# Performance work log

Hardware: AMD Instinct MI355X
Metric: run time of the kernel (lower is better)

Reference implementation:

```python
import jax, jax.numpy as jnp
import numpy as np

N_NODES = 50000
N_EDGES = 640000
IN_DIM = 128
HID = 128
OUT_DIM = 16
BATCH = 2
EPS = 1e-5


def setup_inputs() -> dict:
    key = jax.random.key(0)
    ks = jax.random.split(key, 12)
    x = jax.random.normal(ks[0], (BATCH, N_NODES, IN_DIM), dtype=jnp.float32)
    edge_index = jax.random.randint(ks[1], (2, N_EDGES), 0, N_NODES, dtype=jnp.int32)
    # learned per-edge log-weights (initialized ~0 like nn.Parameter(zeros), small noise for a nontrivial test)
    edge_weight_param = 0.01 * jax.random.normal(ks[2], (N_EDGES,), dtype=jnp.float32)
    s1 = 1.0 / np.sqrt(IN_DIM)
    s2 = 1.0 / np.sqrt(HID)
    W1 = jax.random.uniform(ks[3], (IN_DIM, HID), minval=-s1, maxval=s1, dtype=jnp.float32)
    b1 = jnp.zeros((HID,), jnp.float32)
    W2 = jax.random.uniform(ks[4], (HID, HID), minval=-s2, maxval=s2, dtype=jnp.float32)
    b2 = jnp.zeros((HID,), jnp.float32)
    g1 = jnp.ones((HID,), jnp.float32); be1 = jnp.zeros((HID,), jnp.float32)
    g2 = jnp.ones((HID,), jnp.float32); be2 = jnp.zeros((HID,), jnp.float32)
    Wc = jax.random.uniform(ks[5], (HID, OUT_DIM), minval=-s2, maxval=s2, dtype=jnp.float32)
    bc = jax.random.uniform(ks[6], (OUT_DIM,), minval=-s2, maxval=s2, dtype=jnp.float32)
    return {"x": x, "edge_index": edge_index, "edge_weight_param": edge_weight_param,
            "W1": W1, "b1": b1, "W2": W2, "b2": b2,
            "g1": g1, "be1": be1, "g2": g2, "be2": be2,
            "Wc": Wc, "bc": bc}


def _gcn_norm(edge_index, edge_weight):
    # PyG GCNConv: add self-loops (weight 1), symmetric D^-1/2 A D^-1/2 normalization
    row = jnp.concatenate([edge_index[0], jnp.arange(N_NODES, dtype=edge_index.dtype)])
    col = jnp.concatenate([edge_index[1], jnp.arange(N_NODES, dtype=edge_index.dtype)])
    ew = jnp.concatenate([edge_weight, jnp.ones((N_NODES,), edge_weight.dtype)])
    deg = jax.ops.segment_sum(ew, col, num_segments=N_NODES)
    dinv = jnp.where(deg > 0, jax.lax.rsqrt(jnp.maximum(deg, 1e-30)), 0.0)
    norm = dinv[row] * ew * dinv[col]
    return row, col, norm


def _gcn_conv(x, W, b, row, col, norm):
    # x: [B, N, F_in] -> [B, N, F_out]; gather-scale-scatter over edges
    xw = x @ W                                   # [B, N, H]
    msg = xw[:, row, :] * norm[None, :, None]    # [B, E+N, H]
    out = jax.vmap(lambda m: jax.ops.segment_sum(m, col, num_segments=N_NODES))(msg)
    return out + b


def _batchnorm(h, gamma, beta):
    # training-mode BN over flattened (B*N) rows, biased variance, eps=1e-5
    B, N, F = h.shape
    hf = h.reshape(-1, F)
    mu = hf.mean(axis=0)
    var = hf.var(axis=0)
    return (((hf - mu) * jax.lax.rsqrt(var + EPS)) * gamma + beta).reshape(B, N, F)


def reference(x, edge_index, edge_weight_param, W1, b1, W2, b2, g1, be1, g2, be2, Wc, bc):
    edge_weight = jnp.exp(edge_weight_param)  # learned exp edge weights
    row, col, norm = _gcn_norm(edge_index, edge_weight)
    h = jax.nn.relu(_gcn_conv(x, W1, b1, row, col, norm))
    h = _batchnorm(h, g1, be1)
    # dropout is identity in eval / deterministic reference
    h = jax.nn.relu(_gcn_conv(h, W2, b2, row, col, norm))
    h = _batchnorm(h, g2, be2)
    return h @ Wc + bc  # [B, N, OUT_DIM]
```

## Files before the change

### kernel.cpp

```cpp
#include <hip/hip_runtime.h>
#include <hip/hip_bf16.h>
#include <cstdint>
#include <cstddef>

#define N_NODES 50000
#define N_EDGES 640000
#define ROWS    100000
#define HID     128
#define OUTD    16
#define AGG_BLOCKS 2048
#define MID_BLOCKS 32
#define SCAN_BLOCKS 196
#define GEMM_BLOCKS 512
#define G2_BLOCKS   800
#define GEMM_TILES  (ROWS / 16)
#define PAIR_TILES  (N_NODES / 16)
#define EG_BLOCKS   3500
#define EG_GEMM_WAVES 4000

typedef __attribute__((ext_vector_type(8))) uint16_t ushort8;
typedef __attribute__((ext_vector_type(8))) __bf16   bf16x8;
typedef __attribute__((ext_vector_type(4))) float    floatx4;

union FragU { ushort8 u; bf16x8 b; };

__device__ __forceinline__ float bf_lo(uint32_t u){
  union { uint32_t u; float f; } c; c.u = u << 16; return c.f;
}
__device__ __forceinline__ float bf_hi(uint32_t u){
  union { uint32_t u; float f; } c; c.u = u & 0xffff0000u; return c.f;
}
__device__ __forceinline__ uint16_t f2bf(float f){
  union { float f; uint32_t u; } c; c.f = f;
  uint32_t u = c.u;
  uint32_t r = (u + 0x7fffu + ((u >> 16) & 1u)) >> 16;
  return (uint16_t)r;
}

__device__ __forceinline__ void pack_w(int t, const float* __restrict__ W,
                                       const float* sca ,
                                       uint16_t* __restrict__ WP){
  int L = t & 63;
  int s = (t >> 6) & 3;
  int c = t >> 8;
  int n = (c >> 1) * 32 + 2 * (L & 15) + (c & 1);
  int k0 = s * 32 + (L >> 4) * 8;
  ushort8 r;
#pragma unroll
  for (int j = 0; j < 8; j++){
    float w = W[(size_t)(k0 + j) * HID + n];
    if (sca) w *= sca[k0 + j];
    r[j] = f2bf(w);
  }
  *((ushort8*)(WP + (size_t)t * 8)) = r;
}

__global__ void k_initpack(unsigned long long* __restrict__ dc,
                           const float* __restrict__ W1, uint16_t* __restrict__ WP1){
  int b = blockIdx.x;
  if (b < SCAN_BLOCKS){
    int i = b * 256 + threadIdx.x;
    if (i < N_NODES) dc[i] = 0ull;
  } else {
    pack_w((b - SCAN_BLOCKS) * 256 + threadIdx.x, W1, nullptr, WP1);
  }
}

__global__ __launch_bounds__(256, 2) void k_edge_gemm1(const int* __restrict__ ei,
                                                       const float* __restrict__ ewp,
                                                       unsigned long long* __restrict__ dc,
                                                       unsigned int* __restrict__ slot,
                                                       const float* __restrict__ X,
                                                       const uint16_t* __restrict__ WP,
                                                       uint16_t* __restrict__ Y){
  const int b = blockIdx.x;
  const int g = b % 7;
  if (g < 5){
    const int eb = (b / 7) * 5 + g;
    const int e = eb * 256 + threadIdx.x;
    float w = expf(ewp[e]);
    int c = ei[N_EDGES + e];
    unsigned long long inc = (1ull << 44) | (unsigned long long)(w * 1048576.0f + 0.5f);
    unsigned long long old = atomicAdd(&dc[c], inc);
    slot[e] = (unsigned int)(old >> 44);
    return;
  }
  const int lane = threadIdx.x & 63;
  const int wid  = threadIdx.x >> 6;
  const int gw   = ((b / 7) * 2 + (g - 5)) * 4 + wid;
  const int m    = lane & 15;
  const int kq   = lane >> 4;

  FragU wf[8][4];
#pragma unroll
  for (int c = 0; c < 8; c++)
#pragma unroll
    for (int s = 0; s < 4; s++)
      wf[c][s].u = *((const ushort8*)(WP + (size_t)(((c * 4 + s) * 64 + lane) * 8)));

  unsigned long long* Yq = (unsigned long long*)Y;
  for (int t = gw; t < PAIR_TILES; t += EG_GEMM_WAVES){
    const int nb = t * 16;
    uint32_t pr0[16];
    {
      FragU af[4];
#pragma unroll
      for (int s = 0; s < 4; s++){
        const float* p = X + (size_t)(nb + m) * HID + s * 32 + kq * 8;
        floatx4 f0 = *((const floatx4*)p);
        floatx4 f1 = *((const floatx4*)(p + 4));
        ushort8 r;
#pragma unroll
        for (int j = 0; j < 4; j++){ r[j] = f2bf(f0[j]); r[j + 4] = f2bf(f1[j]); }
        af[s].u = r;
      }
      floatx4 acc[8];
#pragma unroll
      for (int c = 0; c < 8; c++) acc[c] = floatx4{0.f, 0.f, 0.f, 0.f};
#pragma unroll
      for (int s = 0; s < 4; s++)
#pragma unroll
        for (int c = 0; c < 8; c++)
          acc[c] = __builtin_amdgcn_mfma_f32_16x16x32_bf16(af[s].b, wf[c][s].b, acc[c], 0, 0, 0);
#pragma unroll
      for (int t4 = 0; t4 < 4; t4++)
#pragma unroll
        for (int i = 0; i < 4; i++)
          pr0[t4 * 4 + i] = (uint32_t)f2bf(acc[2 * t4][i]) | ((uint32_t)f2bf(acc[2 * t4 + 1][i]) << 16);
    }
    {
      FragU af[4];
#pragma unroll
      for (int s = 0; s < 4; s++){
        const float* p = X + (size_t)(N_NODES + nb + m) * HID + s * 32 + kq * 8;
        floatx4 f0 = *((const floatx4*)p);
        floatx4 f1 = *((const floatx4*)(p + 4));
        ushort8 r;
#pragma unroll
        for (int j = 0; j < 4; j++){ r[j] = f2bf(f0[j]); r[j + 4] = f2bf(f1[j]); }
        af[s].u = r;
      }
      floatx4 acc[8];
#pragma unroll
      for (int c = 0; c < 8; c++) acc[c] = floatx4{0.f, 0.f, 0.f, 0.f};
#pragma unroll
      for (int s = 0; s < 4; s++)
#pragma unroll
        for (int c = 0; c < 8; c++)
          acc[c] = __builtin_amdgcn_mfma_f32_16x16x32_bf16(af[s].b, wf[c][s].b, acc[c], 0, 0, 0);
#pragma unroll
      for (int t4 = 0; t4 < 4; t4++)
#pragma unroll
        for (int i = 0; i < 4; i++){
          uint32_t pr1 = (uint32_t)f2bf(acc[2 * t4][i]) | ((uint32_t)f2bf(acc[2 * t4 + 1][i]) << 16);
          Yq[(size_t)(nb + kq * 4 + i) * 64 + t4 * 16 + m] =
              (unsigned long long)pr0[t4 * 4 + i] | ((unsigned long long)pr1 << 32);
        }
    }
  }
}

__global__ void k_scan_bsum(const unsigned long long* __restrict__ dc, int* __restrict__ bsum,
                            float* __restrict__ dinv){
  __shared__ int sd[256];
  int tid = threadIdx.x;
  int i = blockIdx.x * 256 + tid;
  int cnt = 0;
  if (i < N_NODES){
    unsigned long long v = dc[i];
    cnt = (int)(v >> 44);
    float deg = 1.0f + (float)((double)(v & ((1ull << 44) - 1)) * (1.0 / 1048576.0));
    dinv[i] = 1.0f / sqrtf(deg);
  }
  sd[tid] = cnt;
  __syncthreads();
  for (int off = 128; off > 0; off >>= 1){
    if (tid < off) sd[tid] += sd[tid + off];
    __syncthreads();
  }
  if (tid == 0) bsum[blockIdx.x] = sd[0];
}

__global__ void k_scan_write(const unsigned long long* __restrict__ dc, const int* __restrict__ bsum,
                             int* __restrict__ rp){
  __shared__ int sb[256];
  __shared__ int sd[256];
  int tid = threadIdx.x;
  sb[tid] = (tid < SCAN_BLOCKS && tid < blockIdx.x) ? bsum[tid] : 0;
  __syncthreads();
  for (int off = 128; off > 0; off >>= 1){
    if (tid < off) sb[tid] += sb[tid + off];
    __syncthreads();
  }
  const int base = sb[0];

  int i = blockIdx.x * 256 + tid;
  int v = (i < N_NODES) ? (int)(dc[i] >> 44) : 0;
  sd[tid] = v;
  __syncthreads();
  for (int off = 1; off < 256; off <<= 1){
    int t = (tid >= off) ? sd[tid - off] : 0;
    __syncthreads();
    sd[tid] += t;
    __syncthreads();
  }
  if (i < N_NODES) rp[i] = base + sd[tid] - v;
  if (blockIdx.x == 0 && tid == 0) rp[N_NODES] = N_EDGES;
}

__global__ void k_fill(const int* __restrict__ ei, const float* __restrict__ ewp,
                       const float* __restrict__ dinv, const unsigned int* __restrict__ slot,
                       const int* __restrict__ rp, unsigned long long* __restrict__ edg){
  int e = blockIdx.x * 256 + threadIdx.x;
  if (e < N_EDGES){
    int r = ei[e];
    int c = ei[N_EDGES + e];
    float w = expf(ewp[e]);
    float nrm = dinv[r] * w * dinv[c];
    int p = rp[c] + (int)slot[e];
    edg[p] = ((unsigned long long)__float_as_uint(nrm) << 32) | (unsigned int)r;
  }
}

__global__ __launch_bounds__(256, 2) void k_gemm2(const uint16_t* __restrict__ X,
                                                  const uint16_t* __restrict__ WP,
                                                  uint16_t* __restrict__ Y){
  const int lane = threadIdx.x & 63;
  const int wid  = threadIdx.x >> 6;
  const int gw   = blockIdx.x * 4 + wid;
  const int nw   = G2_BLOCKS * 4;
  const int m    = lane & 15;
  const int kq   = lane >> 4;

  FragU wf[8][4];
#pragma unroll
  for (int c = 0; c < 8; c++)
#pragma unroll
    for (int s = 0; s < 4; s++)
      wf[c][s].u = *((const ushort8*)(WP + (size_t)(((c * 4 + s) * 64 + lane) * 8)));

  unsigned long long* Yq = (unsigned long long*)Y;
  for (int t = gw; t < PAIR_TILES; t += nw){
    const int nb = t * 16;
    uint32_t pr0[16];
    {
      FragU af[4];
#pragma unroll
      for (int s = 0; s < 4; s++)
        af[s].u = *((const ushort8*)(X + (size_t)(nb + m) * HID + s * 32 + kq * 8));
      floatx4 acc[8];
#pragma unroll
      for (int c = 0; c < 8; c++) acc[c] = floatx4{0.f, 0.f, 0.f, 0.f};
#pragma unroll
      for (int s = 0; s < 4; s++)
#pragma unroll
        for (int c = 0; c < 8; c++)
          acc[c] = __builtin_amdgcn_mfma_f32_16x16x32_bf16(af[s].b, wf[c][s].b, acc[c], 0, 0, 0);
#pragma unroll
      for (int t4 = 0; t4 < 4; t4++)
#pragma unroll
        for (int i = 0; i < 4; i++)
          pr0[t4 * 4 + i] = (uint32_t)f2bf(acc[2 * t4][i]) | ((uint32_t)f2bf(acc[2 * t4 + 1][i]) << 16);
    }
    {
      FragU af[4];
#pragma unroll
      for (int s = 0; s < 4; s++)
        af[s].u = *((const ushort8*)(X + (size_t)(N_NODES + nb + m) * HID + s * 32 + kq * 8));
      floatx4 acc[8];
#pragma unroll
      for (int c = 0; c < 8; c++) acc[c] = floatx4{0.f, 0.f, 0.f, 0.f};
#pragma unroll
      for (int s = 0; s < 4; s++)
#pragma unroll
        for (int c = 0; c < 8; c++)
          acc[c] = __builtin_amdgcn_mfma_f32_16x16x32_bf16(af[s].b, wf[c][s].b, acc[c], 0, 0, 0);
#pragma unroll
      for (int t4 = 0; t4 < 4; t4++)
#pragma unroll
        for (int i = 0; i < 4; i++){
          uint32_t pr1 = (uint32_t)f2bf(acc[2 * t4][i]) | ((uint32_t)f2bf(acc[2 * t4 + 1][i]) << 16);
          Yq[(size_t)(nb + kq * 4 + i) * 64 + t4 * 16 + m] =
              (unsigned long long)pr0[t4 * 4 + i] | ((unsigned long long)pr1 << 32);
        }
    }
  }
}

__global__ __launch_bounds__(256) void k_cls_mfma(const uint16_t* __restrict__ H,
                                                  const uint16_t* __restrict__ WPC,
                                                  const float* __restrict__ cvec,
                                                  float* __restrict__ out){
  const int lane = threadIdx.x & 63;
  const int wid  = threadIdx.x >> 6;
  const int gw   = blockIdx.x * 4 + wid;
  const int nw   = GEMM_BLOCKS * 4;
  const int m    = lane & 15;
  const int kq   = lane >> 4;

  FragU wf[4];
#pragma unroll
  for (int s = 0; s < 4; s++)
    wf[s].u = *((const ushort8*)(WPC + (size_t)((s * 64 + lane) * 8)));
  const float cv = cvec[m];

  for (int t = gw; t < GEMM_TILES; t += nw){
    const int row0 = t * 16;
    FragU af[4];
#pragma unroll
    for (int s = 0; s < 4; s++)
      af[s].u = *((const ushort8*)(H + (size_t)(row0 + m) * HID + s * 32 + kq * 8));
    floatx4 acc = floatx4{0.f, 0.f, 0.f, 0.f};
#pragma unroll
    for (int s = 0; s < 4; s++)
      acc = __builtin_amdgcn_mfma_f32_16x16x32_bf16(af[s].b, wf[s].b, acc, 0, 0, 0);
#pragma unroll
    for (int i = 0; i < 4; i++)
      out[(size_t)(row0 + kq * 4 + i) * OUTD + m] = acc[i] + cv;
  }
}

__global__ __launch_bounds__(256) void k_agg(const uint16_t* __restrict__ XW,
                                             const int* __restrict__ rp,
                                             const unsigned long long* __restrict__ edg,
                                             const float* __restrict__ dinv,
                                             const float* __restrict__ bias,
                                             const float* __restrict__ cvec,
                                             uint16_t* __restrict__ H,
                                             float* __restrict__ psum,
                                             float* __restrict__ pssq){
  __shared__ float lsum[128];
  __shared__ float lssq[128];
  const int tid = threadIdx.x;
  if (tid < 128){ lsum[tid] = 0.f; lssq[tid] = 0.f; }
  __syncthreads();

  const int lane = tid & 63;
  const int wid  = tid >> 6;
  const int gw   = blockIdx.x * 4 + wid;
  const int nw   = AGG_BLOCKS * 4;
  const unsigned long long* Xq = (const unsigned long long*)XW;
  uint32_t* Hu = (uint32_t*)H;
  const int f0 = lane * 2;
  const float b0 = bias[f0], b1 = bias[f0 + 1];
  const float c0 = cvec ? cvec[f0] : 0.f;
  const float c1 = cvec ? cvec[f0 + 1] : 0.f;
  float ts0 = 0.f, ts1 = 0.f, tq0 = 0.f, tq1 = 0.f;
  const int lu = lane & 7;

  int node = gw;
  if (node < N_NODES){
    int e0 = rp[node], e1 = rp[node + 1];
    float di = dinv[node];
    unsigned long long sv = Xq[(size_t)node * 64 + lane];
    unsigned long long rec = 0ull;
    if (e0 < e1){
      int a = e0 + lu; if (a > N_EDGES - 1) a = N_EDGES - 1;
      rec = edg[a];
    }
    while (true){
      const int nn = node + nw;
      const bool more = (nn < N_NODES);
      int ne0 = 0, ne1 = 0; float ndi = 0.f; unsigned long long nsv = 0ull;
      if (more){
        ne0 = rp[nn]; ne1 = rp[nn + 1];
        ndi = dinv[nn];
        nsv = Xq[(size_t)nn * 64 + lane];
      }

      const float sn = di * di;
      const uint32_t s0 = (uint32_t)sv, s1 = (uint32_t)(sv >> 32);
      float a0x = sn * bf_lo(s0), a0y = sn * bf_hi(s0);
      float a1x = sn * bf_lo(s1), a1y = sn * bf_hi(s1);
      float wsum = sn;

      for (int e = e0; e < e1; e += 8){
        const int r = e1 - e;
        const uint32_t rlo = (uint32_t)rec;
        const uint32_t rhi = (uint32_t)(rec >> 32);
        const int pe = (r > 8) ? (e + 8) : (more ? ne0 : -1);
        if (pe >= 0){
          int a = pe + lu; if (a > N_EDGES - 1) a = N_EDGES - 1;
          rec = edg[a];
        }
        unsigned long long q[8];
        if (r >= 8){
#pragma unroll
          for (int u = 0; u < 8; u++)
            q[u] = Xq[(size_t)(uint32_t)__builtin_amdgcn_readlane((int)rlo, u) * 64 + lane];
#pragma unroll
          for (int u = 0; u < 8; u++){
            const float w = __uint_as_float((uint32_t)__builtin_amdgcn_readlane((int)rhi, u));
            const uint32_t g0 = (uint32_t)q[u], g1 = (uint32_t)(q[u] >> 32);
            a0x = fmaf(w, bf_lo(g0), a0x); a0y = fmaf(w, bf_hi(g0), a0y);
            a1x = fmaf(w, bf_lo(g1), a1x); a1y = fmaf(w, bf_hi(g1), a1y);
            wsum += w;
          }
        } else {
#pragma unroll
          for (int u = 0; u < 8; u++)
            if (u < r)
              q[u] = Xq[(size_t)(uint32_t)__builtin_amdgcn_readlane((int)rlo, u) * 64 + lane];
#pragma unroll
          for (int u = 0; u < 8; u++)
            if (u < r){
              const float w = __uint_as_float((uint32_t)__builtin_amdgcn_readlane((int)rhi, u));
              const uint32_t g0 = (uint32_t)q[u], g1 = (uint32_t)(q[u] >> 32);
              a0x = fmaf(w, bf_lo(g0), a0x); a0y = fmaf(w, bf_hi(g0), a0y);
              a1x = fmaf(w, bf_lo(g1), a1x); a1y = fmaf(w, bf_hi(g1), a1y);
              wsum += w;
            }
        }
      }
      if (e0 == e1 && more){
        int a = ne0 + lu; if (a > N_EDGES - 1) a = N_EDGES - 1;
        rec = edg[a];
      }

      a0x = fmaxf(fmaf(wsum, c0, a0x) + b0, 0.f); a0y = fmaxf(fmaf(wsum, c1, a0y) + b1, 0.f);
      a1x = fmaxf(fmaf(wsum, c0, a1x) + b0, 0.f); a1y = fmaxf(fmaf(wsum, c1, a1y) + b1, 0.f);
      Hu[(size_t)node * 64 + lane]             = (uint32_t)f2bf(a0x) | ((uint32_t)f2bf(a0y) << 16);
      Hu[(size_t)(N_NODES + node) * 64 + lane] = (uint32_t)f2bf(a1x) | ((uint32_t)f2bf(a1y) << 16);
      ts0 += a0x + a1x; ts1 += a0y + a1y;
      tq0 += a0x * a0x + a1x * a1x; tq1 += a0y * a0y + a1y * a1y;

      if (!more) break;
      node = nn; e0 = ne0; e1 = ne1; di = ndi; sv = nsv;
    }
  }

  atomicAdd(&lsum[f0],     ts0); atomicAdd(&lsum[f0 + 1], ts1);
  atomicAdd(&lssq[f0],     tq0); atomicAdd(&lssq[f0 + 1], tq1);
  __syncthreads();
  if (tid < 128){
    psum[(size_t)blockIdx.x * 128 + tid] = lsum[tid];
    pssq[(size_t)blockIdx.x * 128 + tid] = lssq[tid];
  }
}

__global__ __launch_bounds__(256) void k_bnmid(const float* __restrict__ psum,
                                               const float* __restrict__ pssq,
                                               float* __restrict__ msum,
                                               float* __restrict__ mssq){
  __shared__ float ss[2][128];
  __shared__ float sq[2][128];
  const int tid = threadIdx.x;
  const int f  = tid & 127;
  const int sl = tid >> 7;
  const int rows_per = AGG_BLOCKS / MID_BLOCKS;
  const int base = blockIdx.x * rows_per;
  float s = 0.f, q = 0.f;
  for (int r = base + sl; r < base + rows_per; r += 2){
    s += psum[(size_t)r * 128 + f];
    q += pssq[(size_t)r * 128 + f];
  }
  ss[sl][f] = s; sq[sl][f] = q;
  __syncthreads();
  if (tid < 128){
    msum[(size_t)blockIdx.x * 128 + tid] = ss[0][tid] + ss[1][tid];
    mssq[(size_t)blockIdx.x * 128 + tid] = sq[0][tid] + sq[1][tid];
  }
}

__device__ __forceinline__ void bn_finalize_lds(const float* __restrict__ msum,
                                                const float* __restrict__ mssq,
                                                const float* __restrict__ gamma,
                                                const float* __restrict__ beta,
                                                float* ssc, float* ssh){
  const int tid = threadIdx.x;
  if (tid < 128){
    float S = 0.f, Q = 0.f;
#pragma unroll
    for (int b = 0; b < MID_BLOCKS; b++){
      S += msum[(size_t)b * 128 + tid];
      Q += mssq[(size_t)b * 128 + tid];
    }
    const float inv = 1.0f / (float)ROWS;
    float mu = S * inv;
    float var = fmaxf(Q * inv - mu * mu, 0.f);
    float rstd = 1.0f / sqrtf(var + 1e-5f);
    float sc = gamma[tid] * rstd;
    ssc[tid] = sc;
    ssh[tid] = fmaf(-mu, sc, beta[tid]);
  }
  __syncthreads();
}

__global__ void k_prep2(const float* __restrict__ msum, const float* __restrict__ mssq,
                        const float* __restrict__ gamma, const float* __restrict__ beta,
                        const float* __restrict__ W2,
                        uint16_t* __restrict__ WP2, float* __restrict__ C2){
  __shared__ float ssc[128];
  __shared__ float ssh[128];
  bn_finalize_lds(msum, mssq, gamma, beta, ssc, ssh);
  if (blockIdx.x < 8){
    pack_w(blockIdx.x * 256 + threadIdx.x, W2, ssc, WP2);
  } else if (threadIdx.x < 128){
    const int j = threadIdx.x;
    float a = 0.f;
    for (int k = 0; k < HID; k++) a = fmaf(ssh[k], W2[(size_t)k * HID + j], a);
    C2[j] = a;
  }
}

__global__ void k_prepc(const float* __restrict__ msum, const float* __restrict__ mssq,
                        const float* __restrict__ gamma, const float* __restrict__ beta,
                        const float* __restrict__ Wc, const float* __restrict__ bc,
                        uint16_t* __restrict__ WPC, float* __restrict__ CVC){
  __shared__ float ssc[128];
  __shared__ float ssh[128];
  bn_finalize_lds(msum, mssq, gamma, beta, ssc, ssh);
  if (blockIdx.x == 0){
    int t = threadIdx.x;
    int L = t & 63;
    int s = t >> 6;
    int n = L & 15;
    int k0 = s * 32 + (L >> 4) * 8;
    ushort8 r;
#pragma unroll
    for (int j = 0; j < 8; j++)
      r[j] = f2bf(ssc[k0 + j] * Wc[(size_t)(k0 + j) * OUTD + n]);
    *((ushort8*)(WPC + (size_t)t * 8)) = r;
  } else if (threadIdx.x < OUTD){
    const int j = threadIdx.x;
    float a = bc[j];
    for (int k = 0; k < HID; k++) a = fmaf(ssh[k], Wc[(size_t)k * OUTD + j], a);
    CVC[j] = a;
  }
}

extern "C" void kernel_launch(void* const* d_in, const int* in_sizes, int n_in,
                              void* d_out, int out_size, void* d_ws, size_t ws_size,
                              hipStream_t stream){
  const float* x   = (const float*)d_in[0];
  const int*   ei  = (const int*)d_in[1];
  const float* ewp = (const float*)d_in[2];
  const float* W1  = (const float*)d_in[3];
  const float* b1  = (const float*)d_in[4];
  const float* W2  = (const float*)d_in[5];
  const float* b2  = (const float*)d_in[6];
  const float* g1  = (const float*)d_in[7];
  const float* be1 = (const float*)d_in[8];
  const float* g2  = (const float*)d_in[9];
  const float* be2 = (const float*)d_in[10];
  const float* Wc  = (const float*)d_in[11];
  const float* bc  = (const float*)d_in[12];
  float* out = (float*)d_out;

  char* wsb = (char*)d_ws;
  size_t off = 0;
  auto give = [&](size_t bytes) -> void* {
    void* p = wsb + off;
    off = (off + bytes + 255) & ~(size_t)255;
    return p;
  };
  uint16_t* XW  = (uint16_t*)give((size_t)ROWS * 128 * 2);
  uint16_t* Hb  = (uint16_t*)give((size_t)ROWS * 128 * 2);
  unsigned long long* DC  = (unsigned long long*)give((size_t)N_NODES * 8);
  unsigned long long* EDG = (unsigned long long*)give((size_t)N_EDGES * 8);
  unsigned int* SLOT = (unsigned int*)give((size_t)N_EDGES * 4);
  float* DINV   = (float*)give((size_t)N_NODES * 4);
  int*   RP     = (int*)give((size_t)(N_NODES + 1) * 4);
  int*   BSUM   = (int*)give(1024);
  float* PSUM   = (float*)give((size_t)AGG_BLOCKS * 128 * 4);
  float* PSSQ   = (float*)give((size_t)AGG_BLOCKS * 128 * 4);
  float* MSUM   = (float*)give((size_t)MID_BLOCKS * 128 * 4);
  float* MSSQ   = (float*)give((size_t)MID_BLOCKS * 128 * 4);
  uint16_t* WP1 = (uint16_t*)give((size_t)HID * HID * 2);
  uint16_t* WP2 = (uint16_t*)give((size_t)HID * HID * 2);
  uint16_t* WPC = (uint16_t*)give((size_t)HID * OUTD * 2);
  float* C2     = (float*)give(512);
  float* CVC    = (float*)give(64);
  (void)ws_size; (void)n_in; (void)in_sizes; (void)out_size;

  k_initpack<<<SCAN_BLOCKS + 8, 256, 0, stream>>>(DC, W1, WP1);
  k_edge_gemm1<<<EG_BLOCKS, 256, 0, stream>>>(ei, ewp, DC, SLOT, x, WP1, XW);
  k_scan_bsum<<<SCAN_BLOCKS, 256, 0, stream>>>(DC, BSUM, DINV);
  k_scan_write<<<SCAN_BLOCKS, 256, 0, stream>>>(DC, BSUM, RP);
  k_fill<<<(N_EDGES + 255) / 256, 256, 0, stream>>>(ei, ewp, DINV, SLOT, RP, EDG);
  k_agg<<<AGG_BLOCKS, 256, 0, stream>>>(XW, RP, EDG, DINV, b1, nullptr, Hb, PSUM, PSSQ);
  k_bnmid<<<MID_BLOCKS, 256, 0, stream>>>(PSUM, PSSQ, MSUM, MSSQ);
  k_prep2<<<9, 256, 0, stream>>>(MSUM, MSSQ, g1, be1, W2, WP2, C2);
  k_gemm2<<<G2_BLOCKS, 256, 0, stream>>>(Hb, WP2, XW);
  k_agg<<<AGG_BLOCKS, 256, 0, stream>>>(XW, RP, EDG, DINV, b2, C2, Hb, PSUM, PSSQ);
  k_bnmid<<<MID_BLOCKS, 256, 0, stream>>>(PSUM, PSSQ, MSUM, MSSQ);
  k_prepc<<<2, 256, 0, stream>>>(MSUM, MSSQ, g2, be2, Wc, bc, WPC, CVC);
  k_cls_mfma<<<GEMM_BLOCKS, 256, 0, stream>>>(Hb, WPC, CVC, out);
}
```

Before: 313.1 us.

## Replace two-pass scan with atomic segment allocation and drop BN mid-reduction kernels

The two-kernel exclusive scan for CSR row pointers becomes a single kernel. Each block scans its counts locally and grabs a base offset with one atomicAdd on a global cursor, storing (count, start) pairs per node. Segments are therefore not in node order, which is still valid because aggregation reads start and count together. The separate BN partial-sum reduction kernels are removed, so each prep kernel's blocks now reduce all 2048 per-block partials directly. This cuts three launches in exchange for more redundant serial reduction work inside the small prep kernels.

```diff
diff --git a/kernel.cpp b/kernel.cpp
--- a/kernel.cpp
+++ b/kernel.cpp
@@ -9,7 +9,6 @@
 #define HID     128
 #define OUTD    16
 #define AGG_BLOCKS 2048
-#define MID_BLOCKS 32
 #define SCAN_BLOCKS 196
 #define GEMM_BLOCKS 512
 #define G2_BLOCKS   800
@@ -56,12 +55,14 @@
 }
 
 __global__ void k_initpack(unsigned long long* __restrict__ dc,
-                           const float* __restrict__ W1, uint16_t* __restrict__ WP1){
+                           const float* __restrict__ W1, uint16_t* __restrict__ WP1,
+                           unsigned int* __restrict__ cursor){
   int b = blockIdx.x;
   if (b < SCAN_BLOCKS){
     int i = b * 256 + threadIdx.x;
     if (i < N_NODES) dc[i] = 0ull;
   } else {
+    if (b == SCAN_BLOCKS && threadIdx.x == 0) *cursor = 0u;
     pack_w((b - SCAN_BLOCKS) * 256 + threadIdx.x, W1, nullptr, WP1);
   }
 }
@@ -160,11 +161,14 @@
   }
 }
 
-__global__ void k_scan_bsum(const unsigned long long* __restrict__ dc, int* __restrict__ bsum,
-                            float* __restrict__ dinv){
+__global__ void k_alloc(const unsigned long long* __restrict__ dc,
+                        unsigned long long* __restrict__ rp2,
+                        float* __restrict__ dinv,
+                        unsigned int* __restrict__ cursor){
   __shared__ int sd[256];
-  int tid = threadIdx.x;
-  int i = blockIdx.x * 256 + tid;
+  __shared__ unsigned int sbase;
+  const int tid = threadIdx.x;
+  const int i = blockIdx.x * 256 + tid;
   int cnt = 0;
   if (i < N_NODES){
     unsigned long long v = dc[i];
@@ -174,50 +178,31 @@
   }
   sd[tid] = cnt;
   __syncthreads();
-  for (int off = 128; off > 0; off >>= 1){
-    if (tid < off) sd[tid] += sd[tid + off];
-    __syncthreads();
-  }
-  if (tid == 0) bsum[blockIdx.x] = sd[0];
-}
-
-__global__ void k_scan_write(const unsigned long long* __restrict__ dc, const int* __restrict__ bsum,
-                             int* __restrict__ rp){
-  __shared__ int sb[256];
-  __shared__ int sd[256];
-  int tid = threadIdx.x;
-  sb[tid] = (tid < SCAN_BLOCKS && tid < blockIdx.x) ? bsum[tid] : 0;
-  __syncthreads();
-  for (int off = 128; off > 0; off >>= 1){
-    if (tid < off) sb[tid] += sb[tid + off];
-    __syncthreads();
-  }
-  const int base = sb[0];
-
-  int i = blockIdx.x * 256 + tid;
-  int v = (i < N_NODES) ? (int)(dc[i] >> 44) : 0;
-  sd[tid] = v;
-  __syncthreads();
   for (int off = 1; off < 256; off <<= 1){
     int t = (tid >= off) ? sd[tid - off] : 0;
     __syncthreads();
     sd[tid] += t;
     __syncthreads();
   }
-  if (i < N_NODES) rp[i] = base + sd[tid] - v;
-  if (blockIdx.x == 0 && tid == 0) rp[N_NODES] = N_EDGES;
+  if (tid == 255) sbase = atomicAdd(cursor, (unsigned int)sd[255]);
+  __syncthreads();
+  if (i < N_NODES){
+    unsigned int start = sbase + (unsigned int)(sd[tid] - cnt);
+    rp2[i] = ((unsigned long long)(unsigned int)cnt << 32) | start;
+  }
 }
 
 __global__ void k_fill(const int* __restrict__ ei, const float* __restrict__ ewp,
                        const float* __restrict__ dinv, const unsigned int* __restrict__ slot,
-                       const int* __restrict__ rp, unsigned long long* __restrict__ edg){
+                       const unsigned long long* __restrict__ rp2,
+                       unsigned long long* __restrict__ edg){
   int e = blockIdx.x * 256 + threadIdx.x;
   if (e < N_EDGES){
     int r = ei[e];
     int c = ei[N_EDGES + e];
     float w = expf(ewp[e]);
     float nrm = dinv[r] * w * dinv[c];
-    int p = rp[c] + (int)slot[e];
+    int p = (int)(unsigned int)rp2[c] + (int)slot[e];
     edg[p] = ((unsigned long long)__float_as_uint(nrm) << 32) | (unsigned int)r;
   }
 }
@@ -321,7 +306,7 @@
 }
 
 __global__ __launch_bounds__(256) void k_agg(const uint16_t* __restrict__ XW,
-                                             const int* __restrict__ rp,
+                                             const unsigned long long* __restrict__ rp2,
                                              const unsigned long long* __restrict__ edg,
                                              const float* __restrict__ dinv,
                                              const float* __restrict__ bias,
@@ -350,7 +335,8 @@
 
   int node = gw;
   if (node < N_NODES){
-    int e0 = rp[node], e1 = rp[node + 1];
+    unsigned long long rc = rp2[node];
+    int e0 = (int)(unsigned int)rc, e1 = e0 + (int)(rc >> 32);
     float di = dinv[node];
     unsigned long long sv = Xq[(size_t)node * 64 + lane];
     unsigned long long rec = 0ull;
@@ -363,7 +349,8 @@
       const bool more = (nn < N_NODES);
       int ne0 = 0, ne1 = 0; float ndi = 0.f; unsigned long long nsv = 0ull;
       if (more){
-        ne0 = rp[nn]; ne1 = rp[nn + 1];
+        unsigned long long nrc = rp2[nn];
+        ne0 = (int)(unsigned int)nrc; ne1 = ne0 + (int)(nrc >> 32);
         ndi = dinv[nn];
         nsv = Xq[(size_t)nn * 64 + lane];
       }
@@ -438,46 +425,25 @@
   }
 }
 
-__global__ __launch_bounds__(256) void k_bnmid(const float* __restrict__ psum,
-                                               const float* __restrict__ pssq,
-                                               float* __restrict__ msum,
-                                               float* __restrict__ mssq){
-  __shared__ float ss[2][128];
-  __shared__ float sq[2][128];
-  const int tid = threadIdx.x;
-  const int f  = tid & 127;
-  const int sl = tid >> 7;
-  const int rows_per = AGG_BLOCKS / MID_BLOCKS;
-  const int base = blockIdx.x * rows_per;
-  float s = 0.f, q = 0.f;
-  for (int r = base + sl; r < base + rows_per; r += 2){
-    s += psum[(size_t)r * 128 + f];
-    q += pssq[(size_t)r * 128 + f];
-  }
-  ss[sl][f] = s; sq[sl][f] = q;
-  __syncthreads();
-  if (tid < 128){
-    msum[(size_t)blockIdx.x * 128 + tid] = ss[0][tid] + ss[1][tid];
-    mssq[(size_t)blockIdx.x * 128 + tid] = sq[0][tid] + sq[1][tid];
-  }
-}
-
-__device__ __forceinline__ void bn_finalize_lds(const float* __restrict__ msum,
-                                                const float* __restrict__ mssq,
+__device__ __forceinline__ void bn_finalize_lds(const float* __restrict__ psum,
+                                                const float* __restrict__ pssq,
                                                 const float* __restrict__ gamma,
                                                 const float* __restrict__ beta,
                                                 float* ssc, float* ssh){
+  __shared__ float sS[128];
+  __shared__ float sQ[128];
   const int tid = threadIdx.x;
+  const int f = tid & 127;
+  const float* src = (tid < 128) ? psum : pssq;
+  float S = 0.f;
+#pragma unroll 8
+  for (int b = 0; b < AGG_BLOCKS; b++) S += src[(size_t)b * 128 + f];
+  if (tid < 128) sS[f] = S; else sQ[f] = S;
+  __syncthreads();
   if (tid < 128){
-    float S = 0.f, Q = 0.f;
-#pragma unroll
-    for (int b = 0; b < MID_BLOCKS; b++){
-      S += msum[(size_t)b * 128 + tid];
-      Q += mssq[(size_t)b * 128 + tid];
-    }
     const float inv = 1.0f / (float)ROWS;
-    float mu = S * inv;
-    float var = fmaxf(Q * inv - mu * mu, 0.f);
+    float mu = sS[tid] * inv;
+    float var = fmaxf(sQ[tid] * inv - mu * mu, 0.f);
     float rstd = 1.0f / sqrtf(var + 1e-5f);
     float sc = gamma[tid] * rstd;
     ssc[tid] = sc;
@@ -486,13 +452,13 @@
   __syncthreads();
 }
 
-__global__ void k_prep2(const float* __restrict__ msum, const float* __restrict__ mssq,
+__global__ void k_prep2(const float* __restrict__ psum, const float* __restrict__ pssq,
                         const float* __restrict__ gamma, const float* __restrict__ beta,
                         const float* __restrict__ W2,
                         uint16_t* __restrict__ WP2, float* __restrict__ C2){
   __shared__ float ssc[128];
   __shared__ float ssh[128];
-  bn_finalize_lds(msum, mssq, gamma, beta, ssc, ssh);
+  bn_finalize_lds(psum, pssq, gamma, beta, ssc, ssh);
   if (blockIdx.x < 8){
     pack_w(blockIdx.x * 256 + threadIdx.x, W2, ssc, WP2);
   } else if (threadIdx.x < 128){
@@ -503,13 +469,13 @@
   }
 }
 
-__global__ void k_prepc(const float* __restrict__ msum, const float* __restrict__ mssq,
+__global__ void k_prepc(const float* __restrict__ psum, const float* __restrict__ pssq,
                         const float* __restrict__ gamma, const float* __restrict__ beta,
                         const float* __restrict__ Wc, const float* __restrict__ bc,
                         uint16_t* __restrict__ WPC, float* __restrict__ CVC){
   __shared__ float ssc[128];
   __shared__ float ssh[128];
-  bn_finalize_lds(msum, mssq, gamma, beta, ssc, ssh);
+  bn_finalize_lds(psum, pssq, gamma, beta, ssc, ssh);
   if (blockIdx.x == 0){
     int t = threadIdx.x;
     int L = t & 63;
@@ -560,12 +526,10 @@
   unsigned long long* EDG = (unsigned long long*)give((size_t)N_EDGES * 8);
   unsigned int* SLOT = (unsigned int*)give((size_t)N_EDGES * 4);
   float* DINV   = (float*)give((size_t)N_NODES * 4);
-  int*   RP     = (int*)give((size_t)(N_NODES + 1) * 4);
-  int*   BSUM   = (int*)give(1024);
+  unsigned long long* RP2 = (unsigned long long*)give((size_t)N_NODES * 8);
+  unsigned int* CURSOR = (unsigned int*)give(256);
   float* PSUM   = (float*)give((size_t)AGG_BLOCKS * 128 * 4);
   float* PSSQ   = (float*)give((size_t)AGG_BLOCKS * 128 * 4);
-  float* MSUM   = (float*)give((size_t)MID_BLOCKS * 128 * 4);
-  float* MSSQ   = (float*)give((size_t)MID_BLOCKS * 128 * 4);
   uint16_t* WP1 = (uint16_t*)give((size_t)HID * HID * 2);
   uint16_t* WP2 = (uint16_t*)give((size_t)HID * HID * 2);
   uint16_t* WPC = (uint16_t*)give((size_t)HID * OUTD * 2);
@@ -573,17 +537,14 @@
   float* CVC    = (float*)give(64);
   (void)ws_size; (void)n_in; (void)in_sizes; (void)out_size;
 
-  k_initpack<<<SCAN_BLOCKS + 8, 256, 0, stream>>>(DC, W1, WP1);
+  k_initpack<<<SCAN_BLOCKS + 8, 256, 0, stream>>>(DC, W1, WP1, CURSOR);
   k_edge_gemm1<<<EG_BLOCKS, 256, 0, stream>>>(ei, ewp, DC, SLOT, x, WP1, XW);
-  k_scan_bsum<<<SCAN_BLOCKS, 256, 0, stream>>>(DC, BSUM, DINV);
-  k_scan_write<<<SCAN_BLOCKS, 256, 0, stream>>>(DC, BSUM, RP);
-  k_fill<<<(N_EDGES + 255) / 256, 256, 0, stream>>>(ei, ewp, DINV, SLOT, RP, EDG);
-  k_agg<<<AGG_BLOCKS, 256, 0, stream>>>(XW, RP, EDG, DINV, b1, nullptr, Hb, PSUM, PSSQ);
-  k_bnmid<<<MID_BLOCKS, 256, 0, stream>>>(PSUM, PSSQ, MSUM, MSSQ);
-  k_prep2<<<9, 256, 0, stream>>>(MSUM, MSSQ, g1, be1, W2, WP2, C2);
+  k_alloc<<<SCAN_BLOCKS, 256, 0, stream>>>(DC, RP2, DINV, CURSOR);
+  k_fill<<<(N_EDGES + 255) / 256, 256, 0, stream>>>(ei, ewp, DINV, SLOT, RP2, EDG);
+  k_agg<<<AGG_BLOCKS, 256, 0, stream>>>(XW, RP2, EDG, DINV, b1, nullptr, Hb, PSUM, PSSQ);
+  k_prep2<<<9, 256, 0, stream>>>(PSUM, PSSQ, g1, be1, W2, WP2, C2);
   k_gemm2<<<G2_BLOCKS, 256, 0, stream>>>(Hb, WP2, XW);
-  k_agg<<<AGG_BLOCKS, 256, 0, stream>>>(XW, RP, EDG, DINV, b2, C2, Hb, PSUM, PSSQ);
-  k_bnmid<<<MID_BLOCKS, 256, 0, stream>>>(PSUM, PSSQ, MSUM, MSSQ);
-  k_prepc<<<2, 256, 0, stream>>>(MSUM, MSSQ, g2, be2, Wc, bc, WPC, CVC);
+  k_agg<<<AGG_BLOCKS, 256, 0, stream>>>(XW, RP2, EDG, DINV, b2, C2, Hb, PSUM, PSSQ);
+  k_prepc<<<2, 256, 0, stream>>>(PSUM, PSSQ, g2, be2, Wc, bc, WPC, CVC);
   k_cls_mfma<<<GEMM_BLOCKS, 256, 0, stream>>>(Hb, WPC, CVC, out);
 }
```

New measurement: 442.5 us. +41.3%, slower.
